# Optimization experiments

Measured on AMD Instinct MI355X. Metric: run time of the kernel, lower is better.

The kernel has to match this reference:

```python
import jax, jax.numpy as jnp
import numpy as np

N = 50000
E = 400000
IN_DIM = 128
HID = 128
OUT = 128
HEADS = 8
NEG_SLOPE = 0.2  # PyG GATConv default
BN_EPS = 1e-5


def _gat_conv(x, W, a_src, a_dst, b, src, dst, concat):
    """PyG GATConv (eval): self-loops added by caller. x:[N,F], W:[F,H*C], a_*:[H,C]."""
    H, C = a_src.shape
    xW = (x @ W).reshape(N, H, C)                       # [N,H,C]
    es = jnp.sum(xW * a_src[None], axis=-1)             # [N,H]
    ed = jnp.sum(xW * a_dst[None], axis=-1)             # [N,H]
    e = jax.nn.leaky_relu(es[src] + ed[dst], NEG_SLOPE) # [E,H]
    m = jax.ops.segment_max(e, dst, num_segments=N)     # softmax over incoming edges per dst
    ex = jnp.exp(e - m[dst])
    denom = jax.ops.segment_sum(ex, dst, num_segments=N)
    alpha = ex / denom[dst]                             # [E,H]
    out = jax.ops.segment_sum(xW[src] * alpha[:, :, None], dst, num_segments=N)  # [N,H,C]
    out = out.reshape(N, H * C) if concat else out.mean(axis=1)
    return out + b


def _bn_eval(h, g, be, rm, rv):
    return (h - rm) * jax.lax.rsqrt(rv + BN_EPS) * g + be


def setup_inputs() -> dict:
    key = jax.random.key(0)
    ks = jax.random.split(key, 20)
    C1 = HID // HEADS
    f32 = jnp.float32
    inp = {
        "x": jax.random.normal(ks[0], (N, IN_DIM), dtype=f32),
        "edge_index": jax.random.randint(ks[1], (2, E), 0, N, dtype=jnp.int64),
        # GAT layer 1 (in->hid, 8 heads, concat)
        "W1": jax.random.normal(ks[2], (IN_DIM, HEADS * C1), dtype=f32) * 0.05,
        "a_src1": jax.random.normal(ks[3], (HEADS, C1), dtype=f32) * 0.05,
        "a_dst1": jax.random.normal(ks[4], (HEADS, C1), dtype=f32) * 0.05,
        "b1": jnp.zeros((HEADS * C1,), dtype=f32),
        # GAT layer 2 (hid->hid, 8 heads, concat)
        "W2": jax.random.normal(ks[5], (HID, HEADS * C1), dtype=f32) * 0.05,
        "a_src2": jax.random.normal(ks[6], (HEADS, C1), dtype=f32) * 0.05,
        "a_dst2": jax.random.normal(ks[7], (HEADS, C1), dtype=f32) * 0.05,
        "b2": jnp.zeros((HEADS * C1,), dtype=f32),
        # GAT layer 3 (hid->out, 1 head, no concat)
        "W3": jax.random.normal(ks[8], (HID, OUT), dtype=f32) * 0.05,
        "a_src3": jax.random.normal(ks[9], (1, OUT), dtype=f32) * 0.05,
        "a_dst3": jax.random.normal(ks[10], (1, OUT), dtype=f32) * 0.05,
        "b3": jnp.zeros((OUT,), dtype=f32),
        # residual linears
        "R1w": jax.random.normal(ks[11], (IN_DIM, HID), dtype=f32) * 0.05,
        "R1b": jnp.zeros((HID,), dtype=f32),
        "R2w": jax.random.normal(ks[12], (HID, HID), dtype=f32) * 0.05,
        "R2b": jnp.zeros((HID,), dtype=f32),
        "R3w": jax.random.normal(ks[13], (HID, OUT), dtype=f32) * 0.05,
        "R3b": jnp.zeros((OUT,), dtype=f32),
        # batch norms (eval mode: running stats)
        "g1": jnp.ones((HID,), dtype=f32), "be1": jnp.zeros((HID,), dtype=f32),
        "rm1": jnp.zeros((HID,), dtype=f32), "rv1": jnp.ones((HID,), dtype=f32),
        "g2": jnp.ones((HID,), dtype=f32), "be2": jnp.zeros((HID,), dtype=f32),
        "rm2": jnp.zeros((HID,), dtype=f32), "rv2": jnp.ones((HID,), dtype=f32),
    }
    return inp


def reference(x, edge_index, W1, a_src1, a_dst1, b1, W2, a_src2, a_dst2, b2,
              W3, a_src3, a_dst3, b3, R1w, R1b, R2w, R2b, R3w, R3b,
              g1, be1, rm1, rv1, g2, be2, rm2, rv2):
    # PyG GATConv adds self-loops by default
    loops = jnp.arange(N, dtype=edge_index.dtype)
    src = jnp.concatenate([edge_index[0], loops])
    dst = jnp.concatenate([edge_index[1], loops])

    h = _gat_conv(x, W1, a_src1, a_dst1, b1, src, dst, concat=True) + (x @ R1w + R1b)
    h1 = jax.nn.relu(_bn_eval(h, g1, be1, rm1, rv1))  # dropout identity in eval

    h = _gat_conv(h1, W2, a_src2, a_dst2, b2, src, dst, concat=True) + (h1 @ R2w + R2b)
    h2 = jax.nn.relu(_bn_eval(h, g2, be2, rm2, rv2))

    out = _gat_conv(h2, W3, a_src3, a_dst3, b3, src, dst, concat=False) + (h2 @ R3w + R3b)
    return out
```

## Files before the change

kernel.cpp:

```cpp
#include <hip/hip_runtime.h>
#include <hip/hip_bf16.h>
#include <type_traits>

typedef __hip_bfloat16 bf16;
typedef __hip_bfloat162 bf162;
typedef short v8s __attribute__((ext_vector_type(8)));
typedef short v4s __attribute__((ext_vector_type(4)));
typedef float v4f __attribute__((ext_vector_type(4)));

#define CAP 64

__device__ __forceinline__ float lrelu(float x) { return x > 0.f ? x : 0.2f * x; }
__device__ __forceinline__ float b2f(bf16 v) { return __bfloat162float(v); }

__global__ void k_preW(const float* __restrict__ s0, const float* __restrict__ s1,
                       const float* __restrict__ s2, const float* __restrict__ s3,
                       const float* __restrict__ s4, const float* __restrict__ s5,
                       const float* __restrict__ as1, const float* __restrict__ ad1,
                       const float* __restrict__ as2, const float* __restrict__ ad2,
                       const float* __restrict__ as3, const float* __restrict__ ad3,
                       const float* b1, const float* R1b, const float* g1, const float* be1,
                       const float* rm1, const float* rv1,
                       const float* b2, const float* R2b, const float* g2, const float* be2,
                       const float* rm2, const float* rv2,
                       const float* b3, const float* R3b,
                       bf16* __restrict__ wt, float* __restrict__ prm,
                       int* __restrict__ cnt, int N) {
    int b = blockIdx.x;
    int t = threadIdx.x;
    if (b >= 7) {
        int n4 = N * 4;
        int base = ((b - 7) * 256 + t) * 4;
        int4 z = {0, 0, 0, 0};
#pragma unroll
        for (int k = 0; k < 4; ++k)
            if (base + k < n4) ((int4*)cnt)[base + k] = z;
        return;
    }
    if (b == 6) {
        int c = t;
        if (c < 128) {
            float s1v = g1[c] * rsqrtf(rv1[c] + 1e-5f);
            prm[c]       = b1[c] + R1b[c];
            prm[128 + c] = s1v;
            prm[256 + c] = be1[c] - rm1[c] * s1v;
            float s2v = g2[c] * rsqrtf(rv2[c] + 1e-5f);
            prm[384 + c] = b2[c] + R2b[c];
            prm[512 + c] = s2v;
            prm[640 + c] = be2[c] - rm2[c] * s2v;
            prm[768 + c] = b3[c] + R3b[c];
        }
        return;
    }
    const float* src;
    switch (b) {
        case 0: src = s0; break; case 1: src = s1; break; case 2: src = s2; break;
        case 3: src = s3; break; case 4: src = s4; break; default: src = s5; break;
    }
    bf16* dst = wt + (size_t)b * 18432;
    for (int i = t; i < 16384; i += 256) {
        int k = i >> 7, n = i & 127;
        dst[n * 128 + k] = __float2bfloat16(src[i]);
    }
    if ((b & 1) == 0) {
        int layer = b >> 1;
        if (layer < 2) {
            const float* asr = (layer == 0) ? as1 : as2;
            const float* ads = (layer == 0) ? ad1 : ad2;
            for (int i = t; i < 2048; i += 256) {
                int row = i >> 7, k = i & 127, h = row & 7;
                const float* av = (row < 8) ? asr : ads;
                float s = 0.f;
#pragma unroll
                for (int c = 0; c < 16; ++c) s += src[k * 128 + h * 16 + c] * av[h * 16 + c];
                dst[(128 + row) * 128 + k] = __float2bfloat16(s);
            }
        } else {
            for (int i = t; i < 2048; i += 256) {
                int row = i >> 7, k = i & 127;
                float s = 0.f;
                if (row == 0 || row == 8) {
                    const float* av = (row == 0) ? as3 : ad3;
                    for (int c = 0; c < 128; ++c) s += src[k * 128 + c] * av[c];
                }
                dst[(128 + row) * 128 + k] = __float2bfloat16(s);
            }
        }
    } else {
        for (int i = t; i < 2048; i += 256)
            dst[16384 + i] = __float2bfloat16(0.f);
    }
}

template <typename T>
__device__ __forceinline__ void gemm_body(const T* __restrict__ A,
                                          const bf16* __restrict__ BT0, const bf16* __restrict__ BT1,
                                          bf16* __restrict__ O0, bf16* __restrict__ O1,
                                          float* __restrict__ esed, float* __restrict__ es,
                                          float* __restrict__ ed,
                                          int mode, int nrows, int job, int ntiles,
                                          bf16* Bsh) {
    const int y = (job >= ntiles) ? 1 : 0;
    const int tile = y ? job - ntiles : job;
    const bf16* BT = y ? BT1 : BT0;
    bf16* O = y ? O1 : O0;
    const int t = threadIdx.x;
    const int rowbase = tile * 128;
    const int wave = t >> 6, lane = t & 63, quad = lane >> 4, l16 = lane & 15;

    int gr[2], grc[2];
    gr[0] = rowbase + wave * 32 + l16;      grc[0] = gr[0] < nrows ? gr[0] : nrows - 1;
    gr[1] = gr[0] + 16;                     grc[1] = gr[1] < nrows ? gr[1] : nrows - 1;
    v8s afr[2][4];
    if constexpr (std::is_same<T, float>::value) {
#pragma unroll
        for (int rt = 0; rt < 2; ++rt) {
            const float* arow = A + (size_t)grc[rt] * 128 + quad * 8;
#pragma unroll
            for (int kit = 0; kit < 4; ++kit) {
                float4 u = *(const float4*)(arow + kit * 32);
                float4 w = *(const float4*)(arow + kit * 32 + 4);
                union { bf16 h[8]; v8s v; } tmp;
                tmp.h[0] = __float2bfloat16(u.x); tmp.h[1] = __float2bfloat16(u.y);
                tmp.h[2] = __float2bfloat16(u.z); tmp.h[3] = __float2bfloat16(u.w);
                tmp.h[4] = __float2bfloat16(w.x); tmp.h[5] = __float2bfloat16(w.y);
                tmp.h[6] = __float2bfloat16(w.z); tmp.h[7] = __float2bfloat16(w.w);
                afr[rt][kit] = tmp.v;
            }
        }
    } else {
#pragma unroll
        for (int rt = 0; rt < 2; ++rt) {
            const bf16* arow = A + (size_t)grc[rt] * 128 + quad * 8;
#pragma unroll
            for (int kit = 0; kit < 4; ++kit)
                afr[rt][kit] = *(const v8s*)(arow + kit * 32);
        }
    }

    for (int s = t; s < 288; s += 256) {
        int r = s >> 1, hf = s & 1;
        const float4* bsrc = (const float4*)(BT + r * 128 + hf * 64);
#pragma unroll
        for (int j = 0; j < 8; ++j) {
            int c = hf * 8 + j, cp = c ^ (r & 7);
            *(float4*)(&Bsh[r * 128 + cp * 8]) = bsrc[j];
        }
    }
    __syncthreads();

    v4f acc[2][9];
#pragma unroll
    for (int i = 0; i < 2; ++i)
#pragma unroll
        for (int j = 0; j < 9; ++j) acc[i][j] = (v4f){0.f, 0.f, 0.f, 0.f};
#pragma unroll
    for (int kit = 0; kit < 4; ++kit) {
        v8s bfr[9];
#pragma unroll
        for (int ct = 0; ct < 9; ++ct) {
            int nn = ct * 16 + l16;
            int cp = (kit * 4 + quad) ^ (nn & 7);
            bfr[ct] = *(const v8s*)(&Bsh[nn * 128 + cp * 8]);
        }
#pragma unroll
        for (int rt = 0; rt < 2; ++rt)
#pragma unroll
            for (int ct = 0; ct < 9; ++ct)
                acc[rt][ct] = __builtin_amdgcn_mfma_f32_16x16x32_bf16(bfr[ct], afr[rt][kit], acc[rt][ct], 0, 0, 0);
    }
#pragma unroll
    for (int rt = 0; rt < 2; ++rt) {
        if (gr[rt] < nrows) {
            bf16* orow = O + (size_t)gr[rt] * 128 + quad * 4;
#pragma unroll
            for (int ct = 0; ct < 8; ++ct) {
                union { bf16 h[4]; v4s v; } pk;
#pragma unroll
                for (int r = 0; r < 4; ++r) pk.h[r] = __float2bfloat16(acc[rt][ct][r]);
                *(v4s*)(orow + ct * 16) = pk.v;
            }
            if (mode == 1 && y == 0) {
                *(v4f*)(esed + (size_t)gr[rt] * 16 + quad * 4) = acc[rt][8];
            } else if (mode == 2 && y == 0) {
                if (quad == 0) es[gr[rt]] = acc[rt][8][0];
                else if (quad == 2) ed[gr[rt]] = acc[rt][8][0];
            }
        }
    }
}

__global__ void k_fillgemm(const float* __restrict__ A,
                           const bf16* __restrict__ BT0, const bf16* __restrict__ BT1,
                           bf16* __restrict__ O0, bf16* __restrict__ O1,
                           float* __restrict__ esed, float* __restrict__ es, float* __restrict__ ed,
                           int nrows, int ntiles, int fb,
                           const int* __restrict__ ei, int* __restrict__ cnt,
                           int* __restrict__ csr, int E) {
    __shared__ bf16 Bsh[144 * 128];
    if (blockIdx.x < fb) {
        int base = blockIdx.x * 1024 + threadIdx.x * 4;
        if (base >= E) return;
        if (((E & 3) == 0) && base + 3 < E) {
            int4 s4 = *(const int4*)(ei + base);
            int4 d4 = *(const int4*)(ei + E + base);
            int p0 = atomicAdd(&cnt[(size_t)d4.x * 16], 1);
            int p1 = atomicAdd(&cnt[(size_t)d4.y * 16], 1);
            int p2 = atomicAdd(&cnt[(size_t)d4.z * 16], 1);
            int p3 = atomicAdd(&cnt[(size_t)d4.w * 16], 1);
            if (p0 < 15) cnt[(size_t)d4.x * 16 + 1 + p0] = s4.x;
            else if (p0 < CAP) csr[d4.x * CAP + p0] = s4.x;
            if (p1 < 15) cnt[(size_t)d4.y * 16 + 1 + p1] = s4.y;
            else if (p1 < CAP) csr[d4.y * CAP + p1] = s4.y;
            if (p2 < 15) cnt[(size_t)d4.z * 16 + 1 + p2] = s4.z;
            else if (p2 < CAP) csr[d4.z * CAP + p2] = s4.z;
            if (p3 < 15) cnt[(size_t)d4.w * 16 + 1 + p3] = s4.w;
            else if (p3 < CAP) csr[d4.w * CAP + p3] = s4.w;
        } else {
            for (int i = base; i < E && i < base + 4; ++i) {
                int d = ei[E + i];
                int pos = atomicAdd(&cnt[(size_t)d * 16], 1);
                if (pos < 15) cnt[(size_t)d * 16 + 1 + pos] = ei[i];
                else if (pos < CAP) csr[d * CAP + pos] = ei[i];
            }
        }
        return;
    }
    gemm_body<float>(A, BT0, BT1, O0, O1, esed, es, ed, 1, nrows, blockIdx.x - fb, ntiles, Bsh);
}

__global__ void k_gemm(const bf16* __restrict__ A,
                       const bf16* __restrict__ BT0, const bf16* __restrict__ BT1,
                       bf16* __restrict__ O0, bf16* __restrict__ O1,
                       float* __restrict__ esed, float* __restrict__ es, float* __restrict__ ed,
                       int mode, int nrows, int ntiles) {
    __shared__ bf16 Bsh[144 * 128];
    gemm_body<bf16>(A, BT0, BT1, O0, O1, esed, es, ed, mode, nrows, blockIdx.x, ntiles, Bsh);
}

__global__ void k_agg8(const bf16* __restrict__ xW, const float* __restrict__ esed,
                       const int* __restrict__ cnt, const int* __restrict__ csr,
                       const bf16* __restrict__ rres, const float* __restrict__ prm,
                       bf16* __restrict__ hout, int n) {
    int wave = threadIdx.x >> 6, lane = threadIdx.x & 63;
    int node = blockIdx.x * 4 + wave;
    if (node >= n) return;
    const int g = lane >> 4, l16 = lane & 15;
    const int c0 = l16 * 8;
    const int hc = l16 >> 1;
    const int he = lane & 7;
    float edw = esed[(size_t)node * 16 + 8 + he];
    float wselfh = __expf(lrelu(esed[(size_t)node * 16 + he] + edw));
    float acc[8]; float den = 0.f;
    v8s rv;
#pragma unroll
    for (int i = 0; i < 8; ++i) acc[i] = 0.f;
    {
        float ws = __shfl(wselfh, hc);
        if (g == 0) {
            rv = *(const v8s*)(rres + (size_t)node * 128 + c0);
            v8s xv = *(const v8s*)(xW + (size_t)node * 128 + c0);
            const bf16* xb = (const bf16*)&xv;
            den = ws;
#pragma unroll
            for (int i = 0; i < 8; ++i) acc[i] = ws * b2f(xb[i]);
        }
    }
    int deg = cnt[(size_t)node * 16]; if (deg > CAP) deg = CAP;
    int idx = node;
    if (lane < deg)
        idx = (lane < 15) ? cnt[(size_t)node * 16 + 1 + lane] : csr[(size_t)node * CAP + lane];
    for (int sub = 0; sub * 8 < deg; ++sub) {
        int j0 = sub * 8 + g, j1 = sub * 8 + 4 + g;
        int sv0 = __shfl(idx, j0);
        int sv1 = __shfl(idx, j1);
        v8s xv0 = *(const v8s*)(xW + (size_t)sv0 * 128 + c0);
        v8s xv1 = *(const v8s*)(xW + (size_t)sv1 * 128 + c0);
        int e = sub * 8 + (lane >> 3);
        int sidx = __shfl(idx, e);
        float esv = esed[(size_t)sidx * 16 + he];
        float w = (e < deg) ? __expf(lrelu(esv + edw)) : 0.f;
        float w0 = __shfl(w, g * 8 + hc);
        float w1 = __shfl(w, (4 + g) * 8 + hc);
        const bf16* xb0 = (const bf16*)&xv0;
        const bf16* xb1 = (const bf16*)&xv1;
        den += w0 + w1;
#pragma unroll
        for (int i = 0; i < 8; ++i) acc[i] += w0 * b2f(xb0[i]) + w1 * b2f(xb1[i]);
    }
    den += __shfl_xor(den, 16); den += __shfl_xor(den, 32);
#pragma unroll
    for (int i = 0; i < 8; ++i) {
        acc[i] += __shfl_xor(acc[i], 16);
        acc[i] += __shfl_xor(acc[i], 32);
    }
    if (g == 0) {
        float inv = 1.f / den;
        const bf16* rb = (const bf16*)&rv;
        bf16 outv[8];
#pragma unroll
        for (int i = 0; i < 8; ++i) {
            int c = c0 + i;
            float v = acc[i] * inv + prm[c] + b2f(rb[i]);
            v = fmaxf(v * prm[128 + c] + prm[256 + c], 0.f);
            outv[i] = __float2bfloat16(v);
        }
        *(v8s*)(hout + (size_t)node * 128 + c0) = *(v8s*)outv;
    }
}

__global__ void k_agg1(const bf16* __restrict__ xW, const float* __restrict__ es,
                       const float* __restrict__ ed,
                       const int* __restrict__ cnt, const int* __restrict__ csr,
                       const bf16* __restrict__ rres, const float* __restrict__ bias,
                       float* __restrict__ out, int n) {
    int wave = threadIdx.x >> 6, lane = threadIdx.x & 63;
    int node = blockIdx.x * 4 + wave;
    if (node >= n) return;
    const int g = lane >> 4, l16 = lane & 15;
    const int c0 = l16 * 8;
    float edv = ed[node];
    float wself = __expf(lrelu(es[node] + edv));
    float acc[8]; float den = 0.f;
    v8s rv;
#pragma unroll
    for (int i = 0; i < 8; ++i) acc[i] = 0.f;
    if (g == 0) {
        rv = *(const v8s*)(rres + (size_t)node * 128 + c0);
        v8s xv = *(const v8s*)(xW + (size_t)node * 128 + c0);
        const bf16* xb = (const bf16*)&xv;
        den = wself;
#pragma unroll
        for (int i = 0; i < 8; ++i) acc[i] = wself * b2f(xb[i]);
    }
    int deg = cnt[(size_t)node * 16]; if (deg > CAP) deg = CAP;
    int idx = node;
    if (lane < deg)
        idx = (lane < 15) ? cnt[(size_t)node * 16 + 1 + lane] : csr[(size_t)node * CAP + lane];
    float w = (lane < deg) ? __expf(lrelu(es[idx] + edv)) : 0.f;
    for (int j = 0; j < deg; j += 4) {
        int jl = j + g;
        int sv = __shfl(idx, jl);
        float wj = __shfl(w, jl);
        if (jl >= deg) wj = 0.f;
        v8s xv = *(const v8s*)(xW + (size_t)sv * 128 + c0);
        const bf16* xb = (const bf16*)&xv;
        den += wj;
#pragma unroll
        for (int i = 0; i < 8; ++i) acc[i] += wj * b2f(xb[i]);
    }
    den += __shfl_xor(den, 16); den += __shfl_xor(den, 32);
#pragma unroll
    for (int i = 0; i < 8; ++i) {
        acc[i] += __shfl_xor(acc[i], 16);
        acc[i] += __shfl_xor(acc[i], 32);
    }
    if (g == 0) {
        float inv = 1.f / den;
        const bf16* rb = (const bf16*)&rv;
        float ov[8];
#pragma unroll
        for (int i = 0; i < 8; ++i)
            ov[i] = acc[i] * inv + bias[c0 + i] + b2f(rb[i]);
        float4 o0, o1;
        o0.x = ov[0]; o0.y = ov[1]; o0.z = ov[2]; o0.w = ov[3];
        o1.x = ov[4]; o1.y = ov[5]; o1.z = ov[6]; o1.w = ov[7];
        *(float4*)(out + (size_t)node * 128 + c0) = o0;
        *(float4*)(out + (size_t)node * 128 + c0 + 4) = o1;
    }
}

extern "C" void kernel_launch(void* const* d_in, const int* in_sizes, int n_in,
                              void* d_out, int out_size, void* d_ws, size_t ws_size,
                              hipStream_t stream) {
    const float* x   = (const float*)d_in[0];
    const int*   ei  = (const int*)d_in[1];
    const float* W1  = (const float*)d_in[2];
    const float* as1 = (const float*)d_in[3];
    const float* ad1 = (const float*)d_in[4];
    const float* b1  = (const float*)d_in[5];
    const float* W2  = (const float*)d_in[6];
    const float* as2 = (const float*)d_in[7];
    const float* ad2 = (const float*)d_in[8];
    const float* b2  = (const float*)d_in[9];
    const float* W3  = (const float*)d_in[10];
    const float* as3 = (const float*)d_in[11];
    const float* ad3 = (const float*)d_in[12];
    const float* b3  = (const float*)d_in[13];
    const float* R1w = (const float*)d_in[14];
    const float* R1b = (const float*)d_in[15];
    const float* R2w = (const float*)d_in[16];
    const float* R2b = (const float*)d_in[17];
    const float* R3w = (const float*)d_in[18];
    const float* R3b = (const float*)d_in[19];
    const float* g1  = (const float*)d_in[20];
    const float* be1 = (const float*)d_in[21];
    const float* rm1 = (const float*)d_in[22];
    const float* rv1 = (const float*)d_in[23];
    const float* g2  = (const float*)d_in[24];
    const float* be2 = (const float*)d_in[25];
    const float* rm2 = (const float*)d_in[26];
    const float* rv2 = (const float*)d_in[27];

    const int N = in_sizes[0] / 128;
    const int E = in_sizes[1] / 2;

    char* p = (char*)d_ws;
    size_t off = 0;
    auto alloc = [&](size_t b) { void* r = p + off; off = (off + b + 255) & ~(size_t)255; return r; };
    int*   cnt  = (int*)alloc((size_t)N * 16 * 4);
    int*   csr  = (int*)alloc((size_t)N * CAP * 4);
    bf16*  WT   = (bf16*)alloc((size_t)6 * 18432 * 2);
    float* prm  = (float*)alloc(896 * 4);
    float* esed = (float*)alloc((size_t)N * 16 * 4);
    float* es   = (float*)alloc((size_t)N * 4);
    float* ed   = (float*)alloc((size_t)N * 4);
    bf16*  xW   = (bf16*)alloc((size_t)N * 128 * 2);
    bf16*  rres = (bf16*)alloc((size_t)N * 128 * 2);
    bf16*  hA   = (bf16*)alloc((size_t)N * 128 * 2);
    bf16*  hB   = (bf16*)alloc((size_t)N * 128 * 2);
    (void)ws_size; (void)n_in; (void)out_size;

    const int gx = (N + 127) / 128;
    const int nw = (N + 3) / 4;
    const int fb = (E + 1023) / 1024;
    const int zb = (N * 4 + 1023) / 1024;

    k_preW<<<7 + zb, 256, 0, stream>>>(W1, R1w, W2, R2w, W3, R3w,
                                       as1, ad1, as2, ad2, as3, ad3,
                                       b1, R1b, g1, be1, rm1, rv1,
                                       b2, R2b, g2, be2, rm2, rv2, b3, R3b,
                                       WT, prm, cnt, N);
    k_fillgemm<<<fb + 2 * gx, 256, 0, stream>>>(x, WT, WT + 18432, xW, rres, esed, es, ed,
                                                N, gx, fb, ei, cnt, csr, E);
    k_agg8<<<nw, 256, 0, stream>>>(xW, esed, cnt, csr, rres, prm, hA, N);
    k_gemm<<<2 * gx, 256, 0, stream>>>(hA, WT + 2 * 18432, WT + 3 * 18432, xW, rres, esed, es, ed, 1, N, gx);
    k_agg8<<<nw, 256, 0, stream>>>(xW, esed, cnt, csr, rres, prm + 384, hB, N);
    k_gemm<<<2 * gx, 256, 0, stream>>>(hB, WT + 4 * 18432, WT + 5 * 18432, xW, rres, esed, es, ed, 2, N, gx);
    k_agg1<<<nw, 256, 0, stream>>>(xW, es, ed, cnt, csr, rres, prm + 768, (float*)d_out, N);
}
```

Baseline: 335.8 us.

## Process two row tiles per GEMM block with prefetch; simplify edge bucket storage

```diff
diff --git a/kernel.cpp b/kernel.cpp
--- a/kernel.cpp
+++ b/kernel.cpp
@@ -98,43 +98,43 @@
                                           bf16* __restrict__ O0, bf16* __restrict__ O1,
                                           float* __restrict__ esed, float* __restrict__ es,
                                           float* __restrict__ ed,
-                                          int mode, int nrows, int job, int ntiles,
+                                          int mode, int nrows, int job, int half, int ntiles,
                                           bf16* Bsh) {
-    const int y = (job >= ntiles) ? 1 : 0;
-    const int tile = y ? job - ntiles : job;
+    const int y = (job >= half) ? 1 : 0;
+    const int pair = y ? job - half : job;
+    const int t0 = pair, t1 = pair + half;
     const bf16* BT = y ? BT1 : BT0;
     bf16* O = y ? O1 : O0;
     const int t = threadIdx.x;
-    const int rowbase = tile * 128;
     const int wave = t >> 6, lane = t & 63, quad = lane >> 4, l16 = lane & 15;
 
-    int gr[2], grc[2];
-    gr[0] = rowbase + wave * 32 + l16;      grc[0] = gr[0] < nrows ? gr[0] : nrows - 1;
-    gr[1] = gr[0] + 16;                     grc[1] = gr[1] < nrows ? gr[1] : nrows - 1;
-    v8s afr[2][4];
+    int gr0[2], gc0[2];
+    gr0[0] = t0 * 128 + wave * 32 + l16; gc0[0] = gr0[0] < nrows ? gr0[0] : nrows - 1;
+    gr0[1] = gr0[0] + 16;                gc0[1] = gr0[1] < nrows ? gr0[1] : nrows - 1;
+    v8s afr0[2][4];
     if constexpr (std::is_same<T, float>::value) {
 #pragma unroll
         for (int rt = 0; rt < 2; ++rt) {
-            const float* arow = A + (size_t)grc[rt] * 128 + quad * 8;
+            const float* ar = A + (size_t)gc0[rt] * 128 + quad * 8;
 #pragma unroll
             for (int kit = 0; kit < 4; ++kit) {
-                float4 u = *(const float4*)(arow + kit * 32);
-                float4 w = *(const float4*)(arow + kit * 32 + 4);
+                float4 u = *(const float4*)(ar + kit * 32);
+                float4 w = *(const float4*)(ar + kit * 32 + 4);
                 union { bf16 h[8]; v8s v; } tmp;
                 tmp.h[0] = __float2bfloat16(u.x); tmp.h[1] = __float2bfloat16(u.y);
                 tmp.h[2] = __float2bfloat16(u.z); tmp.h[3] = __float2bfloat16(u.w);
                 tmp.h[4] = __float2bfloat16(w.x); tmp.h[5] = __float2bfloat16(w.y);
                 tmp.h[6] = __float2bfloat16(w.z); tmp.h[7] = __float2bfloat16(w.w);
-                afr[rt][kit] = tmp.v;
+                afr0[rt][kit] = tmp.v;
             }
         }
     } else {
 #pragma unroll
         for (int rt = 0; rt < 2; ++rt) {
-            const bf16* arow = A + (size_t)grc[rt] * 128 + quad * 8;
+            const bf16* ar = A + (size_t)gc0[rt] * 128 + quad * 8;
 #pragma unroll
             for (int kit = 0; kit < 4; ++kit)
-                afr[rt][kit] = *(const v8s*)(arow + kit * 32);
+                afr0[rt][kit] = *(const v8s*)(ar + kit * 32);
         }
     }
 
@@ -148,6 +148,34 @@
         }
     }
     __syncthreads();
+
+    const bool has1 = (t1 < ntiles);
+    int gr1[2], gc1[2];
+    float4 raw[2][8];
+    v8s afr1[2][4];
+    if (has1) {
+        gr1[0] = t1 * 128 + wave * 32 + l16; gc1[0] = gr1[0] < nrows ? gr1[0] : nrows - 1;
+        gr1[1] = gr1[0] + 16;                gc1[1] = gr1[1] < nrows ? gr1[1] : nrows - 1;
+        if constexpr (std::is_same<T, float>::value) {
+#pragma unroll
+            for (int rt = 0; rt < 2; ++rt) {
+                const float* ar = A + (size_t)gc1[rt] * 128 + quad * 8;
+#pragma unroll
+                for (int kit = 0; kit < 4; ++kit) {
+                    raw[rt][kit * 2]     = *(const float4*)(ar + kit * 32);
+                    raw[rt][kit * 2 + 1] = *(const float4*)(ar + kit * 32 + 4);
+                }
+            }
+        } else {
+#pragma unroll
+            for (int rt = 0; rt < 2; ++rt) {
+                const bf16* ar = A + (size_t)gc1[rt] * 128 + quad * 8;
+#pragma unroll
+                for (int kit = 0; kit < 4; ++kit)
+                    afr1[rt][kit] = *(const v8s*)(ar + kit * 32);
+            }
+        }
+    }
 
     v4f acc[2][9];
 #pragma unroll
@@ -167,12 +195,12 @@
         for (int rt = 0; rt < 2; ++rt)
 #pragma unroll
             for (int ct = 0; ct < 9; ++ct)
-                acc[rt][ct] = __builtin_amdgcn_mfma_f32_16x16x32_bf16(bfr[ct], afr[rt][kit], acc[rt][ct], 0, 0, 0);
+                acc[rt][ct] = __builtin_amdgcn_mfma_f32_16x16x32_bf16(bfr[ct], afr0[rt][kit], acc[rt][ct], 0, 0, 0);
     }
 #pragma unroll
     for (int rt = 0; rt < 2; ++rt) {
-        if (gr[rt] < nrows) {
-            bf16* orow = O + (size_t)gr[rt] * 128 + quad * 4;
+        if (gr0[rt] < nrows) {
+            bf16* orow = O + (size_t)gr0[rt] * 128 + quad * 4;
 #pragma unroll
             for (int ct = 0; ct < 8; ++ct) {
                 union { bf16 h[4]; v4s v; } pk;
@@ -181,10 +209,64 @@
                 *(v4s*)(orow + ct * 16) = pk.v;
             }
             if (mode == 1 && y == 0) {
-                *(v4f*)(esed + (size_t)gr[rt] * 16 + quad * 4) = acc[rt][8];
+                *(v4f*)(esed + (size_t)gr0[rt] * 16 + quad * 4) = acc[rt][8];
             } else if (mode == 2 && y == 0) {
-                if (quad == 0) es[gr[rt]] = acc[rt][8][0];
-                else if (quad == 2) ed[gr[rt]] = acc[rt][8][0];
+                if (quad == 0) es[gr0[rt]] = acc[rt][8][0];
+                else if (quad == 2) ed[gr0[rt]] = acc[rt][8][0];
+            }
+        }
+    }
+
+    if (!has1) return;
+    if constexpr (std::is_same<T, float>::value) {
+#pragma unroll
+        for (int rt = 0; rt < 2; ++rt)
+#pragma unroll
+            for (int kit = 0; kit < 4; ++kit) {
+                float4 u = raw[rt][kit * 2], w = raw[rt][kit * 2 + 1];
+                union { bf16 h[8]; v8s v; } tmp;
+                tmp.h[0] = __float2bfloat16(u.x); tmp.h[1] = __float2bfloat16(u.y);
+                tmp.h[2] = __float2bfloat16(u.z); tmp.h[3] = __float2bfloat16(u.w);
+                tmp.h[4] = __float2bfloat16(w.x); tmp.h[5] = __float2bfloat16(w.y);
+                tmp.h[6] = __float2bfloat16(w.z); tmp.h[7] = __float2bfloat16(w.w);
+                afr1[rt][kit] = tmp.v;
+            }
+    }
+#pragma unroll
+    for (int i = 0; i < 2; ++i)
+#pragma unroll
+        for (int j = 0; j < 9; ++j) acc[i][j] = (v4f){0.f, 0.f, 0.f, 0.f};
+#pragma unroll
+    for (int kit = 0; kit < 4; ++kit) {
+        v8s bfr[9];
+#pragma unroll
+        for (int ct = 0; ct < 9; ++ct) {
+            int nn = ct * 16 + l16;
+            int cp = (kit * 4 + quad) ^ (nn & 7);
+            bfr[ct] = *(const v8s*)(&Bsh[nn * 128 + cp * 8]);
+        }
+#pragma unroll
+        for (int rt = 0; rt < 2; ++rt)
+#pragma unroll
+            for (int ct = 0; ct < 9; ++ct)
+                acc[rt][ct] = __builtin_amdgcn_mfma_f32_16x16x32_bf16(bfr[ct], afr1[rt][kit], acc[rt][ct], 0, 0, 0);
+    }
+#pragma unroll
+    for (int rt = 0; rt < 2; ++rt) {
+        if (gr1[rt] < nrows) {
+            bf16* orow = O + (size_t)gr1[rt] * 128 + quad * 4;
+#pragma unroll
+            for (int ct = 0; ct < 8; ++ct) {
+                union { bf16 h[4]; v4s v; } pk;
+#pragma unroll
+                for (int r = 0; r < 4; ++r) pk.h[r] = __float2bfloat16(acc[rt][ct][r]);
+                *(v4s*)(orow + ct * 16) = pk.v;
+            }
+            if (mode == 1 && y == 0) {
+                *(v4f*)(esed + (size_t)gr1[rt] * 16 + quad * 4) = acc[rt][8];
+            } else if (mode == 2 && y == 0) {
+                if (quad == 0) es[gr1[rt]] = acc[rt][8][0];
+                else if (quad == 2) ed[gr1[rt]] = acc[rt][8][0];
             }
         }
     }
@@ -194,48 +276,44 @@
                            const bf16* __restrict__ BT0, const bf16* __restrict__ BT1,
                            bf16* __restrict__ O0, bf16* __restrict__ O1,
                            float* __restrict__ esed, float* __restrict__ es, float* __restrict__ ed,
-                           int nrows, int ntiles, int fb,
+                           int nrows, int half, int ntiles,
                            const int* __restrict__ ei, int* __restrict__ cnt,
                            int* __restrict__ csr, int E) {
     __shared__ bf16 Bsh[144 * 128];
-    if (blockIdx.x < fb) {
-        int base = blockIdx.x * 1024 + threadIdx.x * 4;
-        if (base >= E) return;
-        if (((E & 3) == 0) && base + 3 < E) {
-            int4 s4 = *(const int4*)(ei + base);
-            int4 d4 = *(const int4*)(ei + E + base);
-            int p0 = atomicAdd(&cnt[(size_t)d4.x * 16], 1);
-            int p1 = atomicAdd(&cnt[(size_t)d4.y * 16], 1);
-            int p2 = atomicAdd(&cnt[(size_t)d4.z * 16], 1);
-            int p3 = atomicAdd(&cnt[(size_t)d4.w * 16], 1);
-            if (p0 < 15) cnt[(size_t)d4.x * 16 + 1 + p0] = s4.x;
-            else if (p0 < CAP) csr[d4.x * CAP + p0] = s4.x;
-            if (p1 < 15) cnt[(size_t)d4.y * 16 + 1 + p1] = s4.y;
-            else if (p1 < CAP) csr[d4.y * CAP + p1] = s4.y;
-            if (p2 < 15) cnt[(size_t)d4.z * 16 + 1 + p2] = s4.z;
-            else if (p2 < CAP) csr[d4.z * CAP + p2] = s4.z;
-            if (p3 < 15) cnt[(size_t)d4.w * 16 + 1 + p3] = s4.w;
-            else if (p3 < CAP) csr[d4.w * CAP + p3] = s4.w;
-        } else {
-            for (int i = base; i < E && i < base + 4; ++i) {
-                int d = ei[E + i];
-                int pos = atomicAdd(&cnt[(size_t)d * 16], 1);
-                if (pos < 15) cnt[(size_t)d * 16 + 1 + pos] = ei[i];
-                else if (pos < CAP) csr[d * CAP + pos] = ei[i];
-            }
-        }
+    const int njobs = 2 * half;
+    if (blockIdx.x < njobs) {
+        gemm_body<float>(A, BT0, BT1, O0, O1, esed, es, ed, 1, nrows, blockIdx.x, half, ntiles, Bsh);
         return;
     }
-    gemm_body<float>(A, BT0, BT1, O0, O1, esed, es, ed, 1, nrows, blockIdx.x - fb, ntiles, Bsh);
+    int base = (blockIdx.x - njobs) * 1024 + threadIdx.x * 4;
+    if (base >= E) return;
+    if (((E & 3) == 0) && base + 3 < E) {
+        int4 s4 = *(const int4*)(ei + base);
+        int4 d4 = *(const int4*)(ei + E + base);
+        int p0 = atomicAdd(&cnt[(size_t)d4.x * 16], 1);
+        int p1 = atomicAdd(&cnt[(size_t)d4.y * 16], 1);
+        int p2 = atomicAdd(&cnt[(size_t)d4.z * 16], 1);
+        int p3 = atomicAdd(&cnt[(size_t)d4.w * 16], 1);
+        if (p0 < CAP) csr[d4.x * CAP + p0] = s4.x;
+        if (p1 < CAP) csr[d4.y * CAP + p1] = s4.y;
+        if (p2 < CAP) csr[d4.z * CAP + p2] = s4.z;
+        if (p3 < CAP) csr[d4.w * CAP + p3] = s4.w;
+    } else {
+        for (int i = base; i < E && i < base + 4; ++i) {
+            int d = ei[E + i];
+            int pos = atomicAdd(&cnt[(size_t)d * 16], 1);
+            if (pos < CAP) csr[d * CAP + pos] = ei[i];
+        }
+    }
 }
 
 __global__ void k_gemm(const bf16* __restrict__ A,
                        const bf16* __restrict__ BT0, const bf16* __restrict__ BT1,
                        bf16* __restrict__ O0, bf16* __restrict__ O1,
                        float* __restrict__ esed, float* __restrict__ es, float* __restrict__ ed,
-                       int mode, int nrows, int ntiles) {
+                       int mode, int nrows, int half, int ntiles) {
     __shared__ bf16 Bsh[144 * 128];
-    gemm_body<bf16>(A, BT0, BT1, O0, O1, esed, es, ed, mode, nrows, blockIdx.x, ntiles, Bsh);
+    gemm_body<bf16>(A, BT0, BT1, O0, O1, esed, es, ed, mode, nrows, blockIdx.x, half, ntiles, Bsh);
 }
 
 __global__ void k_agg8(const bf16* __restrict__ xW, const float* __restrict__ esed,
@@ -267,9 +345,8 @@
         }
     }
     int deg = cnt[(size_t)node * 16]; if (deg > CAP) deg = CAP;
-    int idx = node;
-    if (lane < deg)
-        idx = (lane < 15) ? cnt[(size_t)node * 16 + 1 + lane] : csr[(size_t)node * CAP + lane];
+    const int* bucket = csr + (size_t)node * CAP;
+    int idx = (lane < deg) ? bucket[lane] : node;
     for (int sub = 0; sub * 8 < deg; ++sub) {
         int j0 = sub * 8 + g, j1 = sub * 8 + 4 + g;
         int sv0 = __shfl(idx, j0);
@@ -334,9 +411,8 @@
         for (int i = 0; i < 8; ++i) acc[i] = wself * b2f(xb[i]);
     }
     int deg = cnt[(size_t)node * 16]; if (deg > CAP) deg = CAP;
-    int idx = node;
-    if (lane < deg)
-        idx = (lane < 15) ? cnt[(size_t)node * 16 + 1 + lane] : csr[(size_t)node * CAP + lane];
+    const int* bucket = csr + (size_t)node * CAP;
+    int idx = (lane < deg) ? bucket[lane] : node;
     float w = (lane < deg) ? __expf(lrelu(es[idx] + edv)) : 0.f;
     for (int j = 0; j < deg; j += 4) {
         int jl = j + g;
@@ -422,6 +498,8 @@
     (void)ws_size; (void)n_in; (void)out_size;
 
     const int gx = (N + 127) / 128;
+    const int half = (gx + 1) / 2;
+    const int gjobs = 2 * half;
     const int nw = (N + 3) / 4;
     const int fb = (E + 1023) / 1024;
     const int zb = (N * 4 + 1023) / 1024;
@@ -431,11 +509,11 @@
                                        b1, R1b, g1, be1, rm1, rv1,
                                        b2, R2b, g2, be2, rm2, rv2, b3, R3b,
                                        WT, prm, cnt, N);
-    k_fillgemm<<<fb + 2 * gx, 256, 0, stream>>>(x, WT, WT + 18432, xW, rres, esed, es, ed,
-                                                N, gx, fb, ei, cnt, csr, E);
+    k_fillgemm<<<gjobs + fb, 256, 0, stream>>>(x, WT, WT + 18432, xW, rres, esed, es, ed,
+                                               N, half, gx, ei, cnt, csr, E);
     k_agg8<<<nw, 256, 0, stream>>>(xW, esed, cnt, csr, rres, prm, hA, N);
-    k_gemm<<<2 * gx, 256, 0, stream>>>(hA, WT + 2 * 18432, WT + 3 * 18432, xW, rres, esed, es, ed, 1, N, gx);
+    k_gemm<<<gjobs, 256, 0, stream>>>(hA, WT + 2 * 18432, WT + 3 * 18432, xW, rres, esed, es, ed, 1, N, half, gx);
     k_agg8<<<nw, 256, 0, stream>>>(xW, esed, cnt, csr, rres, prm + 384, hB, N);
-    k_gemm<<<2 * gx, 256, 0, stream>>>(hB, WT + 4 * 18432, WT + 5 * 18432, xW, rres, esed, es, ed, 2, N, gx);
+    k_gemm<<<gjobs, 256, 0, stream>>>(hB, WT + 4 * 18432, WT + 5 * 18432, xW, rres, esed, es, ed, 2, N, half, gx);
     k_agg1<<<nw, 256, 0, stream>>>(xW, es, ed, cnt, csr, rres, prm + 768, (float*)d_out, N);
 }
```

New measurement: 387.0 us. +15.2%, slower.

## Read GEMM B fragments directly from global, reorder fused blocks, drop inline edge slots

Applied to the files above, without the earlier changes.

```diff
diff --git a/kernel.cpp b/kernel.cpp
--- a/kernel.cpp
+++ b/kernel.cpp
@@ -98,8 +98,7 @@
                                           bf16* __restrict__ O0, bf16* __restrict__ O1,
                                           float* __restrict__ esed, float* __restrict__ es,
                                           float* __restrict__ ed,
-                                          int mode, int nrows, int job, int ntiles,
-                                          bf16* Bsh) {
+                                          int mode, int nrows, int job, int ntiles) {
     const int y = (job >= ntiles) ? 1 : 0;
     const int tile = y ? job - ntiles : job;
     const bf16* BT = y ? BT1 : BT0;
@@ -108,18 +107,18 @@
     const int rowbase = tile * 128;
     const int wave = t >> 6, lane = t & 63, quad = lane >> 4, l16 = lane & 15;
 
-    int gr[2], grc[2];
-    gr[0] = rowbase + wave * 32 + l16;      grc[0] = gr[0] < nrows ? gr[0] : nrows - 1;
-    gr[1] = gr[0] + 16;                     grc[1] = gr[1] < nrows ? gr[1] : nrows - 1;
+    int gr[2], gc[2];
+    gr[0] = rowbase + wave * 32 + l16; gc[0] = gr[0] < nrows ? gr[0] : nrows - 1;
+    gr[1] = gr[0] + 16;                gc[1] = gr[1] < nrows ? gr[1] : nrows - 1;
     v8s afr[2][4];
     if constexpr (std::is_same<T, float>::value) {
 #pragma unroll
         for (int rt = 0; rt < 2; ++rt) {
-            const float* arow = A + (size_t)grc[rt] * 128 + quad * 8;
+            const float* ar = A + (size_t)gc[rt] * 128 + quad * 8;
 #pragma unroll
             for (int kit = 0; kit < 4; ++kit) {
-                float4 u = *(const float4*)(arow + kit * 32);
-                float4 w = *(const float4*)(arow + kit * 32 + 4);
+                float4 u = *(const float4*)(ar + kit * 32);
+                float4 w = *(const float4*)(ar + kit * 32 + 4);
                 union { bf16 h[8]; v8s v; } tmp;
                 tmp.h[0] = __float2bfloat16(u.x); tmp.h[1] = __float2bfloat16(u.y);
                 tmp.h[2] = __float2bfloat16(u.z); tmp.h[3] = __float2bfloat16(u.w);
@@ -131,44 +130,33 @@
     } else {
 #pragma unroll
         for (int rt = 0; rt < 2; ++rt) {
-            const bf16* arow = A + (size_t)grc[rt] * 128 + quad * 8;
+            const bf16* ar = A + (size_t)gc[rt] * 128 + quad * 8;
 #pragma unroll
             for (int kit = 0; kit < 4; ++kit)
-                afr[rt][kit] = *(const v8s*)(arow + kit * 32);
-        }
-    }
-
-    for (int s = t; s < 288; s += 256) {
-        int r = s >> 1, hf = s & 1;
-        const float4* bsrc = (const float4*)(BT + r * 128 + hf * 64);
-#pragma unroll
-        for (int j = 0; j < 8; ++j) {
-            int c = hf * 8 + j, cp = c ^ (r & 7);
-            *(float4*)(&Bsh[r * 128 + cp * 8]) = bsrc[j];
-        }
-    }
-    __syncthreads();
+                afr[rt][kit] = *(const v8s*)(ar + kit * 32);
+        }
+    }
 
     v4f acc[2][9];
 #pragma unroll
     for (int i = 0; i < 2; ++i)
 #pragma unroll
         for (int j = 0; j < 9; ++j) acc[i][j] = (v4f){0.f, 0.f, 0.f, 0.f};
+
 #pragma unroll
     for (int kit = 0; kit < 4; ++kit) {
+        const bf16* brow = BT + (size_t)l16 * 128 + (kit * 4 + quad) * 8;
         v8s bfr[9];
 #pragma unroll
-        for (int ct = 0; ct < 9; ++ct) {
-            int nn = ct * 16 + l16;
-            int cp = (kit * 4 + quad) ^ (nn & 7);
-            bfr[ct] = *(const v8s*)(&Bsh[nn * 128 + cp * 8]);
-        }
+        for (int ct = 0; ct < 9; ++ct)
+            bfr[ct] = *(const v8s*)(brow + ct * 16 * 128);
 #pragma unroll
         for (int rt = 0; rt < 2; ++rt)
 #pragma unroll
             for (int ct = 0; ct < 9; ++ct)
                 acc[rt][ct] = __builtin_amdgcn_mfma_f32_16x16x32_bf16(bfr[ct], afr[rt][kit], acc[rt][ct], 0, 0, 0);
     }
+
 #pragma unroll
     for (int rt = 0; rt < 2; ++rt) {
         if (gr[rt] < nrows) {
@@ -194,39 +182,34 @@
                            const bf16* __restrict__ BT0, const bf16* __restrict__ BT1,
                            bf16* __restrict__ O0, bf16* __restrict__ O1,
                            float* __restrict__ esed, float* __restrict__ es, float* __restrict__ ed,
-                           int nrows, int ntiles, int fb,
+                           int nrows, int ntiles,
                            const int* __restrict__ ei, int* __restrict__ cnt,
                            int* __restrict__ csr, int E) {
-    __shared__ bf16 Bsh[144 * 128];
-    if (blockIdx.x < fb) {
-        int base = blockIdx.x * 1024 + threadIdx.x * 4;
-        if (base >= E) return;
-        if (((E & 3) == 0) && base + 3 < E) {
-            int4 s4 = *(const int4*)(ei + base);
-            int4 d4 = *(const int4*)(ei + E + base);
-            int p0 = atomicAdd(&cnt[(size_t)d4.x * 16], 1);
-            int p1 = atomicAdd(&cnt[(size_t)d4.y * 16], 1);
-            int p2 = atomicAdd(&cnt[(size_t)d4.z * 16], 1);
-            int p3 = atomicAdd(&cnt[(size_t)d4.w * 16], 1);
-            if (p0 < 15) cnt[(size_t)d4.x * 16 + 1 + p0] = s4.x;
-            else if (p0 < CAP) csr[d4.x * CAP + p0] = s4.x;
-            if (p1 < 15) cnt[(size_t)d4.y * 16 + 1 + p1] = s4.y;
-            else if (p1 < CAP) csr[d4.y * CAP + p1] = s4.y;
-            if (p2 < 15) cnt[(size_t)d4.z * 16 + 1 + p2] = s4.z;
-            else if (p2 < CAP) csr[d4.z * CAP + p2] = s4.z;
-            if (p3 < 15) cnt[(size_t)d4.w * 16 + 1 + p3] = s4.w;
-            else if (p3 < CAP) csr[d4.w * CAP + p3] = s4.w;
-        } else {
-            for (int i = base; i < E && i < base + 4; ++i) {
-                int d = ei[E + i];
-                int pos = atomicAdd(&cnt[(size_t)d * 16], 1);
-                if (pos < 15) cnt[(size_t)d * 16 + 1 + pos] = ei[i];
-                else if (pos < CAP) csr[d * CAP + pos] = ei[i];
-            }
-        }
+    const int njobs = 2 * ntiles;
+    if (blockIdx.x < njobs) {
+        gemm_body<float>(A, BT0, BT1, O0, O1, esed, es, ed, 1, nrows, blockIdx.x, ntiles);
         return;
     }
-    gemm_body<float>(A, BT0, BT1, O0, O1, esed, es, ed, 1, nrows, blockIdx.x - fb, ntiles, Bsh);
+    int base = (blockIdx.x - njobs) * 1024 + threadIdx.x * 4;
+    if (base >= E) return;
+    if (((E & 3) == 0) && base + 3 < E) {
+        int4 s4 = *(const int4*)(ei + base);
+        int4 d4 = *(const int4*)(ei + E + base);
+        int p0 = atomicAdd(&cnt[(size_t)d4.x * 16], 1);
+        int p1 = atomicAdd(&cnt[(size_t)d4.y * 16], 1);
+        int p2 = atomicAdd(&cnt[(size_t)d4.z * 16], 1);
+        int p3 = atomicAdd(&cnt[(size_t)d4.w * 16], 1);
+        if (p0 < CAP) csr[d4.x * CAP + p0] = s4.x;
+        if (p1 < CAP) csr[d4.y * CAP + p1] = s4.y;
+        if (p2 < CAP) csr[d4.z * CAP + p2] = s4.z;
+        if (p3 < CAP) csr[d4.w * CAP + p3] = s4.w;
+    } else {
+        for (int i = base; i < E && i < base + 4; ++i) {
+            int d = ei[E + i];
+            int pos = atomicAdd(&cnt[(size_t)d * 16], 1);
+            if (pos < CAP) csr[d * CAP + pos] = ei[i];
+        }
+    }
 }
 
 __global__ void k_gemm(const bf16* __restrict__ A,
@@ -234,8 +217,7 @@
                        bf16* __restrict__ O0, bf16* __restrict__ O1,
                        float* __restrict__ esed, float* __restrict__ es, float* __restrict__ ed,
                        int mode, int nrows, int ntiles) {
-    __shared__ bf16 Bsh[144 * 128];
-    gemm_body<bf16>(A, BT0, BT1, O0, O1, esed, es, ed, mode, nrows, blockIdx.x, ntiles, Bsh);
+    gemm_body<bf16>(A, BT0, BT1, O0, O1, esed, es, ed, mode, nrows, blockIdx.x, ntiles);
 }
 
 __global__ void k_agg8(const bf16* __restrict__ xW, const float* __restrict__ esed,
@@ -267,9 +249,8 @@
         }
     }
     int deg = cnt[(size_t)node * 16]; if (deg > CAP) deg = CAP;
-    int idx = node;
-    if (lane < deg)
-        idx = (lane < 15) ? cnt[(size_t)node * 16 + 1 + lane] : csr[(size_t)node * CAP + lane];
+    const int* bucket = csr + (size_t)node * CAP;
+    int idx = (lane < deg) ? bucket[lane] : node;
     for (int sub = 0; sub * 8 < deg; ++sub) {
         int j0 = sub * 8 + g, j1 = sub * 8 + 4 + g;
         int sv0 = __shfl(idx, j0);
@@ -334,9 +315,8 @@
         for (int i = 0; i < 8; ++i) acc[i] = wself * b2f(xb[i]);
     }
     int deg = cnt[(size_t)node * 16]; if (deg > CAP) deg = CAP;
-    int idx = node;
-    if (lane < deg)
-        idx = (lane < 15) ? cnt[(size_t)node * 16 + 1 + lane] : csr[(size_t)node * CAP + lane];
+    const int* bucket = csr + (size_t)node * CAP;
+    int idx = (lane < deg) ? bucket[lane] : node;
     float w = (lane < deg) ? __expf(lrelu(es[idx] + edv)) : 0.f;
     for (int j = 0; j < deg; j += 4) {
         int jl = j + g;
@@ -431,8 +411,8 @@
                                        b1, R1b, g1, be1, rm1, rv1,
                                        b2, R2b, g2, be2, rm2, rv2, b3, R3b,
                                        WT, prm, cnt, N);
-    k_fillgemm<<<fb + 2 * gx, 256, 0, stream>>>(x, WT, WT + 18432, xW, rres, esed, es, ed,
-                                                N, gx, fb, ei, cnt, csr, E);
+    k_fillgemm<<<2 * gx + fb, 256, 0, stream>>>(x, WT, WT + 18432, xW, rres, esed, es, ed,
+                                                N, gx, ei, cnt, csr, E);
     k_agg8<<<nw, 256, 0, stream>>>(xW, esed, cnt, csr, rres, prm, hA, N);
     k_gemm<<<2 * gx, 256, 0, stream>>>(hA, WT + 2 * 18432, WT + 3 * 18432, xW, rres, esed, es, ed, 1, N, gx);
     k_agg8<<<nw, 256, 0, stream>>>(xW, esed, cnt, csr, rres, prm + 384, hB, N);
```

Measured after the change: 359.3 us. +7.0%, slower.
